# Optimization experiments

Measured on AMD Instinct MI355X. Metric: run time of the kernel, lower is better.

The kernel has to match this reference:

```python
import jax, jax.numpy as jnp
import numpy as np

VOCAB, H, MAXLEN = 50257, 1024, 128


def setup_inputs() -> dict:
    key = jax.random.key(0)
    ks = jax.random.split(key, 14)
    s = 0.02  # init scale
    f32 = jnp.float32
    return {
        "x": jax.random.randint(ks[0], (1,), 0, VOCAB),
        "h": jax.random.normal(ks[1], (1, 1, H), f32),
        "encoder_outputs": jax.random.normal(ks[2], (MAXLEN, H), f32),
        "emb": jax.random.normal(ks[3], (VOCAB, H), f32) * s,
        "W_attn": jax.random.normal(ks[4], (MAXLEN, 2 * H), f32) * s,
        "b_attn": jnp.zeros((MAXLEN,), f32),
        "W_comb": jax.random.normal(ks[5], (H, 2 * H), f32) * s,
        "b_comb": jnp.zeros((H,), f32),
        "w_ih": jax.random.normal(ks[6], (3 * H, H), f32) * s,
        "w_hh": jax.random.normal(ks[7], (3 * H, H), f32) * s,
        "b_ih": jnp.zeros((3 * H,), f32),
        "b_hh": jnp.zeros((3 * H,), f32),
        "W_out": jax.random.normal(ks[8], (VOCAB, H), f32) * s,
        "b_out": jnp.zeros((VOCAB,), f32),
    }


def reference(x, h, encoder_outputs, emb, W_attn, b_attn, W_comb, b_comb,
              w_ih, w_hh, b_ih, b_hh, W_out, b_out):
    # Single decode step (batch=1, seq=1); dropout in eval mode (identity).
    e = emb[x]                       # [1, H] embedded token
    h0 = h[0]                        # [1, H] hidden state
    # attention over encoder outputs
    attn_w = jax.nn.softmax(jnp.concatenate([e, h0], axis=1) @ W_attn.T + b_attn, axis=1)  # [1, MAXLEN]
    attn_applied = attn_w @ encoder_outputs                                                 # [1, H]
    # combine + relu
    g = jax.nn.relu(jnp.concatenate([e, attn_applied], axis=1) @ W_comb.T + b_comb)        # [1, H]
    # single-step GRU (PyTorch gate order: r, z, n)
    gi = g @ w_ih.T + b_ih           # [1, 3H]
    gh = h0 @ w_hh.T + b_hh          # [1, 3H]
    i_r, i_z, i_n = jnp.split(gi, 3, axis=1)
    h_r, h_z, h_n = jnp.split(gh, 3, axis=1)
    r = jax.nn.sigmoid(i_r + h_r)
    z = jax.nn.sigmoid(i_z + h_z)
    n = jnp.tanh(i_n + r * h_n)
    h_new = (1.0 - z) * n + z * h0   # [1, H]
    out = jax.nn.log_softmax(h_new @ W_out.T + b_out, axis=1)  # [1, VOCAB]
    return out, h_new[None], attn_w
```

## Files before the change

kernel.cpp:

```cpp
#include <hip/hip_runtime.h>
#include <math.h>

#define H 1024
#define MAXLEN 128
#define VOCAB 50257

#define ROWS_PB 16
#define NB_OUT ((VOCAB + ROWS_PB - 1) / ROWS_PB)
#define NB_SUB ((VOCAB + 1023) / 1024)

__device__ inline float wave_reduce_sum(float v) {
    #pragma unroll
    for (int off = 32; off > 0; off >>= 1) v += __shfl_down(v, off);
    return v;
}

__device__ inline float dot4(float4 a, float4 b) {
    return a.x * b.x + a.y * b.y + a.z * b.z + a.w * b.w;
}

__global__ void k_attn_logits(const int* x, const float* h, const float* emb,
                              const float* W_attn, const float* b_attn, float* logits) {
    const int lane = threadIdx.x & 63, wid = threadIdx.x >> 6;
    const int row = blockIdx.x * 4 + wid;
    const float4* w4 = (const float4*)(W_attn + row * (2 * H));
    const float4* e4 = (const float4*)(emb + (long long)x[0] * H);
    const float4* h4 = (const float4*)h;
    float acc = 0.f;
    #pragma unroll
    for (int i = 0; i < 8; i++) {
        int idx = lane + i * 64;
        float4 wv = w4[idx];
        float4 cv = (idx < 256) ? e4[idx] : h4[idx - 256];
        acc += dot4(wv, cv);
    }
    acc = wave_reduce_sum(acc);
    if (lane == 0) logits[row] = acc + b_attn[row];
}

__global__ void k_attn_sm_apply(const float* logits, const float* enc,
                                float* attn_applied, float* out_attn) {
    __shared__ float buf[MAXLEN];
    __shared__ float wsm[MAXLEN];
    int t = threadIdx.x;
    if (t < MAXLEN) buf[t] = logits[t];
    __syncthreads();
    float m = -INFINITY;
    #pragma unroll 8
    for (int k = 0; k < MAXLEN; k++) m = fmaxf(m, buf[k]);
    if (t < MAXLEN) wsm[t] = expf(buf[t] - m);
    __syncthreads();
    float s = 0.f;
    #pragma unroll 8
    for (int k = 0; k < MAXLEN; k++) s += wsm[k];
    float inv = 1.f / s;
    if (t < MAXLEN) {
        int j = blockIdx.x * MAXLEN + t;
        float acc = 0.f;
        #pragma unroll 8
        for (int k = 0; k < MAXLEN; k++) acc += wsm[k] * enc[k * H + j];
        attn_applied[j] = acc * inv;
        if (blockIdx.x == 0) out_attn[t] = wsm[t] * inv;
    }
}

__global__ void k_combine(const int* x, const float* emb, const float* attn_applied,
                          const float* W_comb, const float* b_comb, float* g) {
    int wid = threadIdx.x >> 6, lane = threadIdx.x & 63;
    int row = blockIdx.x * 4 + wid;
    const float4* w4 = (const float4*)(W_comb + (long long)row * (2 * H));
    const float4* e4 = (const float4*)(emb + (long long)x[0] * H);
    const float4* a4 = (const float4*)attn_applied;
    float acc = 0.f;
    #pragma unroll
    for (int i = 0; i < 8; i++) {
        int idx = lane + i * 64;
        float4 wv = w4[idx];
        float4 cv = (idx < 256) ? e4[idx] : a4[idx - 256];
        acc += dot4(wv, cv);
    }
    acc = wave_reduce_sum(acc);
    if (lane == 0) g[row] = fmaxf(acc + b_comb[row], 0.f);
}

__global__ void k_gru_fused(const float* g, const float* h,
                            const float* w_ih, const float* w_hh,
                            const float* b_ih, const float* b_hh, float* h_new) {
    const int j = blockIdx.x, t = threadIdx.x;
    const int lane = t & 63, wid = t >> 6;
    __shared__ float red6[4][6];
    const float4* g4 = (const float4*)g;
    const float4* h4 = (const float4*)h;
    float4 vg = g4[t];
    float4 vh = h4[t];
    float a6[6];
    #pragma unroll
    for (int gt = 0; gt < 3; gt++) {
        const float4* wi = (const float4*)(w_ih + (long long)(j + gt * H) * H);
        const float4* wh = (const float4*)(w_hh + (long long)(j + gt * H) * H);
        a6[gt]     = dot4(wi[t], vg);
        a6[3 + gt] = dot4(wh[t], vh);
    }
    #pragma unroll
    for (int k = 0; k < 6; k++) {
        float v = a6[k];
        #pragma unroll
        for (int off = 32; off > 0; off >>= 1) v += __shfl_down(v, off);
        if (lane == 0) red6[wid][k] = v;
    }
    __syncthreads();
    if (t == 0) {
        float d[6];
        #pragma unroll
        for (int k = 0; k < 6; k++)
            d[k] = red6[0][k] + red6[1][k] + red6[2][k] + red6[3][k];
        float gi_r = d[0] + b_ih[j];
        float gi_z = d[1] + b_ih[j + H];
        float gi_n = d[2] + b_ih[j + 2 * H];
        float gh_r = d[3] + b_hh[j];
        float gh_z = d[4] + b_hh[j + H];
        float gh_n = d[5] + b_hh[j + 2 * H];
        float r = 1.f / (1.f + expf(-(gi_r + gh_r)));
        float z = 1.f / (1.f + expf(-(gi_z + gh_z)));
        float n = tanhf(gi_n + r * gh_n);
        h_new[j] = (1.f - z) * n + z * h[j];
    }
}

__global__ void k_out_matvec(const float* hn, const float* W_out, const float* b_out,
                             float* out, float* pmax, float* psum) {
    const int t = threadIdx.x;
    const int lane = t & 63, wid = t >> 6;
    const int row0 = blockIdx.x * ROWS_PB + wid * 4;
    __shared__ float lm[ROWS_PB];

    const float4* h4 = (const float4*)hn;
    float4 hreg[4];
    #pragma unroll
    for (int i = 0; i < 4; i++) hreg[i] = h4[lane + i * 64];

    float lv[4] = {-INFINITY, -INFINITY, -INFINITY, -INFINITY};
    if (row0 + 3 < VOCAB) {
        float4 a[4][4];
        #pragma unroll
        for (int r = 0; r < 4; r++) {
            const float4* w4 = (const float4*)(W_out + (long long)(row0 + r) * H);
            #pragma unroll
            for (int i = 0; i < 4; i++) a[r][i] = w4[lane + i * 64];
        }
        #pragma unroll
        for (int r = 0; r < 4; r++) {
            float acc = 0.f;
            #pragma unroll
            for (int i = 0; i < 4; i++) acc += dot4(a[r][i], hreg[i]);
            acc = wave_reduce_sum(acc);
            if (lane == 0) {
                lv[r] = acc + b_out[row0 + r];
                out[row0 + r] = lv[r];
            }
        }
    } else {
        for (int r = 0; r < 4; r++) {
            int row = row0 + r;
            if (row >= VOCAB) break;
            const float4* w4 = (const float4*)(W_out + (long long)row * H);
            float acc = 0.f;
            #pragma unroll
            for (int i = 0; i < 4; i++) acc += dot4(w4[lane + i * 64], hreg[i]);
            acc = wave_reduce_sum(acc);
            if (lane == 0) {
                lv[r] = acc + b_out[row];
                out[row] = lv[r];
            }
        }
    }
    if (lane == 0) {
        #pragma unroll
        for (int r = 0; r < 4; r++) lm[wid * 4 + r] = lv[r];
    }
    __syncthreads();
    if (t == 0) {
        float m = -INFINITY;
        #pragma unroll
        for (int i = 0; i < ROWS_PB; i++) m = fmaxf(m, lm[i]);
        float s = 0.f;
        #pragma unroll
        for (int i = 0; i < ROWS_PB; i++)
            if (lm[i] != -INFINITY) s += expf(lm[i] - m);
        pmax[blockIdx.x] = m;
        psum[blockIdx.x] = s;
    }
}

__global__ void k_merge_sub(const float* pmax, const float* psum, float* out) {
    __shared__ float red[16];
    __shared__ float Msh;
    const int t = threadIdx.x;
    const int lane = t & 63, wid = t >> 6;
    float m = -INFINITY;
    for (int i = t; i < NB_OUT; i += 1024) m = fmaxf(m, pmax[i]);
    #pragma unroll
    for (int off = 32; off > 0; off >>= 1) m = fmaxf(m, __shfl_down(m, off));
    if (lane == 0) red[wid] = m;
    __syncthreads();
    if (t == 0) {
        float mm = red[0];
        #pragma unroll
        for (int i = 1; i < 16; i++) mm = fmaxf(mm, red[i]);
        Msh = mm;
    }
    __syncthreads();
    const float M = Msh;
    float s = 0.f;
    for (int i = t; i < NB_OUT; i += 1024) s += psum[i] * expf(pmax[i] - M);
    s = wave_reduce_sum(s);
    __syncthreads();
    if (lane == 0) red[wid] = s;
    __syncthreads();
    if (t == 0) {
        float ss = 0.f;
        #pragma unroll
        for (int i = 0; i < 16; i++) ss += red[i];
        Msh = M + logf(ss);
    }
    __syncthreads();
    const float c = Msh;
    int v = blockIdx.x * 1024 + t;
    if (v < VOCAB) out[v] -= c;
}

extern "C" void kernel_launch(void* const* d_in, const int* in_sizes, int n_in,
                              void* d_out, int out_size, void* d_ws, size_t ws_size,
                              hipStream_t stream) {
    const int*   x     = (const int*)d_in[0];
    const float* h     = (const float*)d_in[1];
    const float* enc   = (const float*)d_in[2];
    const float* emb   = (const float*)d_in[3];
    const float* W_attn= (const float*)d_in[4];
    const float* b_attn= (const float*)d_in[5];
    const float* W_comb= (const float*)d_in[6];
    const float* b_comb= (const float*)d_in[7];
    const float* w_ih  = (const float*)d_in[8];
    const float* w_hh  = (const float*)d_in[9];
    const float* b_ih  = (const float*)d_in[10];
    const float* b_hh  = (const float*)d_in[11];
    const float* W_out = (const float*)d_in[12];
    const float* b_out = (const float*)d_in[13];

    float* out      = (float*)d_out;
    float* out_h    = out + VOCAB;
    float* out_attn = out + VOCAB + H;

    float* ws          = (float*)d_ws;
    float* logits128   = ws;
    float* attn_applied= ws + 256;
    float* g_vec       = ws + 1280;
    float* pmax        = ws + 4096;
    float* psum        = ws + 12288;

    k_attn_logits<<<MAXLEN / 4, 256, 0, stream>>>(x, h, emb, W_attn, b_attn, logits128);
    k_attn_sm_apply<<<H / MAXLEN, 256, 0, stream>>>(logits128, enc, attn_applied, out_attn);
    k_combine<<<H / 4, 256, 0, stream>>>(x, emb, attn_applied, W_comb, b_comb, g_vec);
    k_gru_fused<<<H, 256, 0, stream>>>(g_vec, h, w_ih, w_hh, b_ih, b_hh, out_h);
    k_out_matvec<<<NB_OUT, 256, 0, stream>>>(out_h, W_out, b_out, out, pmax, psum);
    k_merge_sub<<<NB_SUB, 1024, 0, stream>>>(pmax, psum, out);
}
```

Baseline: 69.29 us.

## Fuse attention softmax/apply into combine kernel with per-block redundant recompute

Merges the attention softmax-and-apply kernel into the combine kernel, so each of the 256 blocks recomputes the full attention-weighted encoder sum into shared memory before its combine rows. This removes one kernel launch and the global round trip for the attention vector. In exchange every block re-reads the entire encoder output matrix, multiplying cache traffic and per-block work.

```diff
diff --git a/kernel.cpp b/kernel.cpp
--- a/kernel.cpp
+++ b/kernel.cpp
@@ -38,11 +38,15 @@
     if (lane == 0) logits[row] = acc + b_attn[row];
 }
 
-__global__ void k_attn_sm_apply(const float* logits, const float* enc,
-                                float* attn_applied, float* out_attn) {
+__global__ void k_sm_combine(const int* x, const float* emb, const float* logits,
+                             const float* enc, const float* W_comb, const float* b_comb,
+                             float* g_vec, float* out_attn) {
     __shared__ float buf[MAXLEN];
     __shared__ float wsm[MAXLEN];
-    int t = threadIdx.x;
+    __shared__ float attn[H] __attribute__((aligned(16)));
+    const int t = threadIdx.x;
+    const int lane = t & 63, wid = t >> 6;
+
     if (t < MAXLEN) buf[t] = logits[t];
     __syncthreads();
     float m = -INFINITY;
@@ -53,34 +57,37 @@
     float s = 0.f;
     #pragma unroll 8
     for (int k = 0; k < MAXLEN; k++) s += wsm[k];
-    float inv = 1.f / s;
-    if (t < MAXLEN) {
-        int j = blockIdx.x * MAXLEN + t;
+    const float inv = 1.f / s;
+
+    #pragma unroll
+    for (int jj = 0; jj < 4; jj++) {
+        int j = jj * 256 + t;
         float acc = 0.f;
         #pragma unroll 8
         for (int k = 0; k < MAXLEN; k++) acc += wsm[k] * enc[k * H + j];
-        attn_applied[j] = acc * inv;
-        if (blockIdx.x == 0) out_attn[t] = wsm[t] * inv;
-    }
-}
-
-__global__ void k_combine(const int* x, const float* emb, const float* attn_applied,
-                          const float* W_comb, const float* b_comb, float* g) {
-    int wid = threadIdx.x >> 6, lane = threadIdx.x & 63;
-    int row = blockIdx.x * 4 + wid;
+        attn[j] = acc * inv;
+    }
+    if (blockIdx.x == 0 && t < MAXLEN) out_attn[t] = wsm[t] * inv;
+    __syncthreads();
+
+    const int row = blockIdx.x * 4 + wid;
     const float4* w4 = (const float4*)(W_comb + (long long)row * (2 * H));
     const float4* e4 = (const float4*)(emb + (long long)x[0] * H);
-    const float4* a4 = (const float4*)attn_applied;
+    const float4* a4 = (const float4*)attn;
     float acc = 0.f;
     #pragma unroll
-    for (int i = 0; i < 8; i++) {
+    for (int i = 0; i < 4; i++) {
         int idx = lane + i * 64;
-        float4 wv = w4[idx];
-        float4 cv = (idx < 256) ? e4[idx] : a4[idx - 256];
-        acc += dot4(wv, cv);
+        acc += dot4(w4[idx], e4[idx]);
+    }
+    #pragma unroll
+    for (int i = 4; i < 8; i++) {
+        int idx = lane + i * 64;
+        float4 av = a4[idx - 256];
+        acc += dot4(w4[idx], av);
     }
     acc = wave_reduce_sum(acc);
-    if (lane == 0) g[row] = fmaxf(acc + b_comb[row], 0.f);
+    if (lane == 0) g_vec[row] = fmaxf(acc + b_comb[row], 0.f);
 }
 
 __global__ void k_gru_fused(const float* g, const float* h,
@@ -253,14 +260,13 @@
 
     float* ws          = (float*)d_ws;
     float* logits128   = ws;
-    float* attn_applied= ws + 256;
     float* g_vec       = ws + 1280;
     float* pmax        = ws + 4096;
     float* psum        = ws + 12288;
 
     k_attn_logits<<<MAXLEN / 4, 256, 0, stream>>>(x, h, emb, W_attn, b_attn, logits128);
-    k_attn_sm_apply<<<H / MAXLEN, 256, 0, stream>>>(logits128, enc, attn_applied, out_attn);
-    k_combine<<<H / 4, 256, 0, stream>>>(x, emb, attn_applied, W_comb, b_comb, g_vec);
+    k_sm_combine<<<H / 4, 256, 0, stream>>>(x, emb, logits128, enc,
+                                            W_comb, b_comb, g_vec, out_attn);
     k_gru_fused<<<H, 256, 0, stream>>>(g_vec, h, w_ih, w_hh, b_ih, b_hh, out_h);
     k_out_matvec<<<NB_OUT, 256, 0, stream>>>(out_h, W_out, b_out, out, pmax, psum);
     k_merge_sub<<<NB_SUB, 1024, 0, stream>>>(pmax, psum, out);
```

Result: slower. 86.41 us (+24.7%).
